# Optimization experiments

Hardware: AMD Instinct MI355X
Metric: run time of the kernel (lower is better)

Reference implementation:

```python
import jax, jax.numpy as jnp
import numpy as np

K1, K2, K3 = 6, 4, 3  # knn_graph k (loop=True -> self included, dist 0 is always top)


def _sqdist(a, b):
    # a: [B,N,3], b: [B,M,3] -> [B,N,M] squared euclidean distances
    an = jnp.sum(a * a, -1)[:, :, None]
    bn = jnp.sum(b * b, -1)[:, None, :]
    return an + bn - 2.0 * jnp.einsum('bnd,bmd->bnm', a, b)


def _knn_idx(pos, k):
    # for each point, indices of its k nearest neighbors (self included, loop=True)
    d = _sqdist(pos, pos)                 # [B,N,N]
    _, idx = jax.lax.top_k(-d, k)         # [B,N,k]
    return idx


def _gather(a, idx):
    # a: [B,N,...], idx: [B,...] -> per-cloud gather
    return jax.vmap(lambda ab, ib: ab[ib])(a, idx)


def _fps(pos, m):
    # farthest point sampling on one cloud [N,3], deterministic start at index 0
    min_d = jnp.sum((pos - pos[0]) ** 2, -1)  # [N]

    def step(min_d, _):
        idx = jnp.argmax(min_d)
        d = jnp.sum((pos - pos[idx]) ** 2, -1)
        return jnp.minimum(min_d, d), idx

    _, idxs = jax.lax.scan(step, min_d, None, length=m - 1)
    return jnp.concatenate([jnp.zeros((1,), dtype=idxs.dtype), idxs])


def _pn_layer(h, pos, k, W1, b1, W2, b2):
    # PointNetLayer: gather h_i/h_j/pos_i/pos_j over knn edges, MLP, max-aggregate
    idx = _knn_idx(pos, k)                       # [B,N,k]
    h_j = _gather(h, idx)                        # [B,N,k,C]
    pos_j = _gather(pos, idx)                    # [B,N,k,3]
    rel = pos_j - pos[:, :, None, :]             # pos_j - pos_i
    h_i = jnp.broadcast_to(h[:, :, None, :], h_j.shape)
    inp = jnp.concatenate([h_i, h_j, rel], -1)   # [B,N,k,2C+3]
    msg = jnp.maximum(inp @ W1 + b1, 0.0) @ W2 + b2
    return jnp.max(msg, axis=2)                  # scatter-max == dense max over k


def _forward(x, pos, W11, b11, W12, b12, W21, b21, W22, b22, W31, b31, W32, b32, Wr, br):
    h = jax.nn.relu(_pn_layer(x, pos, K1, W11, b11, W12, b12))
    idx = jax.vmap(lambda p: _fps(p, p.shape[0] // 2))(pos)   # ratio=0.5
    pos, h = _gather(pos, idx), _gather(h, idx)
    h = jax.nn.relu(_pn_layer(h, pos, K2, W21, b21, W22, b22))
    idx = jax.vmap(lambda p: _fps(p, p.shape[0] // 2))(pos)
    pos, h = _gather(pos, idx), _gather(h, idx)
    h = jax.nn.relu(_pn_layer(h, pos, K3, W31, b31, W32, b32))
    g = jnp.max(h, axis=1)                        # global_max_pool
    return g @ Wr + br                            # [B,10]


def _lin(key, fin, fout):
    k1, k2 = jax.random.split(key)
    lim = 1.0 / np.sqrt(fin)
    W = jax.random.uniform(k1, (fin, fout), minval=-lim, maxval=lim, dtype=jnp.float32)
    b = jax.random.uniform(k2, (fout,), minval=-lim, maxval=lim, dtype=jnp.float32)
    return W, b


def setup_inputs() -> dict:
    key = jax.random.key(0)
    ks = jax.random.split(key, 10)
    B, N = 16, 4096
    x = jax.random.normal(ks[0], (B, N, 1), dtype=jnp.float32)
    pos = jax.random.uniform(ks[1], (B, N, 3), dtype=jnp.float32)
    W11, b11 = _lin(ks[2], 1 * 2 + 3, 32)
    W12, b12 = _lin(ks[3], 32, 32)
    W21, b21 = _lin(ks[4], 32 * 2 + 3, 32)
    W22, b22 = _lin(ks[5], 32, 32)
    W31, b31 = _lin(ks[6], 32 * 2 + 3, 32)
    W32, b32 = _lin(ks[7], 32, 32)
    Wr, br = _lin(ks[8], 32, 10)
    return dict(x=x, pos=pos, W11=W11, b11=b11, W12=W12, b12=b12,
                W21=W21, b21=b21, W22=W22, b22=b22,
                W31=W31, b31=b31, W32=W32, b32=b32, Wr=Wr, br=br)


def reference(x, pos, W11, b11, W12, b12, W21, b21, W22, b22, W31, b31, W32, b32, Wr, br):
    return _forward(x, pos, W11, b11, W12, b12, W21, b21, W22, b22,
                    W31, b31, W32, b32, Wr, br)
```

## Files before the change

### kernel.cpp

```cpp
#include <hip/hip_runtime.h>

#define BATCH 16
#define NP1 4096
#define NP2 2048
#define NP3 1024

typedef float v2f __attribute__((ext_vector_type(2)));

__device__ __forceinline__ float f_add(float a, float b) { return __fadd_rn(a, b); }
__device__ __forceinline__ float f_mul(float a, float b) { return __fmul_rn(a, b); }
__device__ __forceinline__ float f_sub(float a, float b) { return __fsub_rn(a, b); }
__device__ __forceinline__ float sqnorm3(float x, float y, float z) {
  return f_add(f_add(f_mul(x, x), f_mul(y, y)), f_mul(z, z));
}

__device__ __forceinline__ unsigned long long u64max(unsigned long long a,
                                                     unsigned long long b) {
  return a > b ? a : b;
}
__device__ __forceinline__ unsigned long long u64min(unsigned long long a,
                                                     unsigned long long b) {
  return a < b ? a : b;
}
__device__ __forceinline__ double dmax(double a, double b) { return __builtin_fmax(a, b); }
__device__ __forceinline__ double dmin(double a, double b) { return __builtin_fmin(a, b); }

template<int CTRL, int RMASK>
__device__ __forceinline__ unsigned long long dpp_u64(unsigned long long k) {
  const int lo = __builtin_amdgcn_update_dpp(0, (int)(unsigned)k, CTRL, RMASK, 0xF, true);
  const int hi = __builtin_amdgcn_update_dpp(0, (int)(unsigned)(k >> 32), CTRL, RMASK, 0xF, true);
  return ((unsigned long long)(unsigned)hi << 32) | (unsigned)lo;
}
template<int CTRL, int RMASK>
__device__ __forceinline__ double dpp_dbl(double v) {
  return __longlong_as_double(
      (long long)dpp_u64<CTRL, RMASK>((unsigned long long)__double_as_longlong(v)));
}


__device__ __forceinline__ void tup_comb(double& a1, double& a2, double b1, double b2) {
  const double hi = dmax(a1, b1);
  const double lo = dmin(a1, b1);
  a2 = dmax(lo, dmax(a2, b2));
  a1 = hi;
}
template<int CTRL, int RMASK>
__device__ __forceinline__ void tup_stage(double& a1, double& a2) {
  const double b1 = dpp_dbl<CTRL, RMASK>(a1);
  const double b2 = dpp_dbl<CTRL, RMASK>(a2);
  tup_comb(a1, a2, b1, b2);
}

template<int N, int M>
__device__ void fps_block(char* __restrict__ smem, const float* __restrict__ P,
                          int* __restrict__ samp, float* __restrict__ pos_out)
{
#pragma clang fp contract(off)
  constexpr int THREADS = 512;
  constexpr int E = N / THREADS;
  constexpr int P2 = E / 2;
  float4* pos4 = (float4*)smem;
  unsigned short* ord = (unsigned short*)(smem + 16 * N);
  int* sampL = (int*)(smem + 18 * N);
  unsigned* cursor = (unsigned*)(smem + 18 * N + 4 * M);
  double* kslots = (double*)(smem + 18 * N + 4 * M + 32);
  const int tid = threadIdx.x;
  const int lane = tid & 63, wv = tid >> 6;
  const int myslot = lane & 7;
  if (tid < 8) cursor[tid] = 0u;
  __syncthreads();
  int oct[E];
#pragma unroll
  for (int e = 0; e < E; ++e) {
    const int t = e * THREADS + tid;
    const float x = P[t * 3], y = P[t * 3 + 1], z = P[t * 3 + 2];
    pos4[t] = make_float4(x, y, z, 0.f);
    oct[e] = (x > 0.5f ? 1 : 0) | (y > 0.5f ? 2 : 0) | (z > 0.5f ? 4 : 0);
    atomicAdd(&cursor[oct[e]], 1u);
  }
  __syncthreads();
  if (tid == 0) {
    unsigned run = 0;
#pragma unroll
    for (int o = 0; o < 8; ++o) { const unsigned c = cursor[o]; cursor[o] = run; run += c; }
  }
  __syncthreads();
#pragma unroll
  for (int e = 0; e < E; ++e) {
    const unsigned d = atomicAdd(&cursor[oct[e]], 1u);
    ord[d] = (unsigned short)(e * THREADS + tid);
  }
  __syncthreads();
  const float4 p0 = pos4[0];
  const float x0 = p0.x, y0 = p0.y, z0 = p0.z;
  v2f X2[P2], Y2[P2], Z2[P2], MD2[P2];
  unsigned ILO[E];
  float mnx = 1e30f, mny = 1e30f, mnz = 1e30f;
  float mxx = -1e30f, mxy = -1e30f, mxz = -1e30f;
  {
    const v2f x0v = {x0, x0}, y0v = {y0, y0}, z0v = {z0, z0};
#pragma unroll
    for (int p = 0; p < P2; ++p) {
      const int q0 = wv * (64 * E) + (2 * p) * 64 + lane;
      const int o0 = ord[q0], o1 = ord[q0 + 64];
      const float4 a0 = pos4[o0], a1 = pos4[o1];
      X2[p] = (v2f){a0.x, a1.x}; Y2[p] = (v2f){a0.y, a1.y}; Z2[p] = (v2f){a0.z, a1.z};
      mnx = fminf(mnx, fminf(a0.x, a1.x)); mxx = fmaxf(mxx, fmaxf(a0.x, a1.x));
      mny = fminf(mny, fminf(a0.y, a1.y)); mxy = fmaxf(mxy, fmaxf(a0.y, a1.y));
      mnz = fminf(mnz, fminf(a0.z, a1.z)); mxz = fmaxf(mxz, fmaxf(a0.z, a1.z));
      const v2f dx = X2[p] - x0v, dy = Y2[p] - y0v, dz = Z2[p] - z0v;
      MD2[p] = (dx * dx + dy * dy) + dz * dz;
      ILO[2 * p]     = 0xFFFFFFFFu - (unsigned)o0;
      ILO[2 * p + 1] = 0xFFFFFFFFu - (unsigned)o1;
    }
  }
#pragma unroll
  for (int off = 1; off < 64; off <<= 1) {
    mnx = fminf(mnx, __shfl_xor(mnx, off)); mxx = fmaxf(mxx, __shfl_xor(mxx, off));
    mny = fminf(mny, __shfl_xor(mny, off)); mxy = fmaxf(mxy, __shfl_xor(mxy, off));
    mnz = fminf(mnz, __shfl_xor(mnz, off)); mxz = fmaxf(mxz, __shfl_xor(mxz, off));
  }
  if (tid == 0) sampL[0] = 0;
  bool dirty = true;
  double W1 = 0.0, W2 = 0.0;
  int s = 1, it = 0;
#pragma unroll 1
  while (s < M) {
    if (dirty) {
      double k[E];
#pragma unroll
      for (int p = 0; p < P2; ++p) {
        k[2 * p] = __longlong_as_double((long long)(
            ((unsigned long long)__float_as_uint(MD2[p].x) << 32) | ILO[2 * p]));
        k[2 * p + 1] = __longlong_as_double((long long)(
            ((unsigned long long)__float_as_uint(MD2[p].y) << 32) | ILO[2 * p + 1]));
      }
      double A1 = dmax(k[0], k[1]), A2 = dmin(k[0], k[1]);
      double B1 = dmax(k[2], k[3]), B2 = dmin(k[2], k[3]);
      double C1 = dmax(k[4], k[5]), C2 = dmin(k[4], k[5]);
      double D1 = dmax(k[6], k[7]), D2 = dmin(k[6], k[7]);
      tup_comb(A1, A2, B1, B2); tup_comb(C1, C2, D1, D2); tup_comb(A1, A2, C1, C2);
      tup_stage<0x111, 0xF>(A1, A2);
      tup_stage<0x112, 0xF>(A1, A2);
      tup_stage<0x114, 0xF>(A1, A2);
      tup_stage<0x118, 0xF>(A1, A2);
      tup_stage<0x142, 0xA>(A1, A2);
      tup_stage<0x143, 0xC>(A1, A2);
      W1 = A1; W2 = A2;
    }
    const int pb = it & 1;
    if (lane == 63) ((double2*)kslots)[pb * 8 + wv] = make_double2(W1, W2);
    __syncthreads();
    double2 tt = ((double2*)kslots)[pb * 8 + myslot];
    double T1 = tt.x, T2 = tt.y;
    tup_stage<0xB1, 0xF>(T1, T2);
    tup_stage<0x4E, 0xF>(T1, T2);
    tup_stage<0x124, 0xF>(T1, T2);
    const unsigned long long g1b = (unsigned long long)__double_as_longlong(T1);
    const unsigned long long g2b = (unsigned long long)__double_as_longlong(T2);
    const int gi1 = (int)(0xFFFFFFFFu - (unsigned)g1b);
    const int gi2 = (int)(0xFFFFFFFFu - (unsigned)g2b);
    const float4 sp1 = pos4[gi1];
    const float4 sp2 = pos4[gi2];
    const float md2b = __uint_as_float((unsigned)(g2b >> 32));
    const float ddx = f_sub(sp2.x, sp1.x), ddy = f_sub(sp2.y, sp1.y),
                ddz = f_sub(sp2.z, sp1.z);
    const float dchk = f_add(f_add(f_mul(ddx, ddx), f_mul(ddy, ddy)), f_mul(ddz, ddz));
    const bool take2 = (s + 1 < M) && (dchk >= md2b);
    if (tid == 0) { sampL[s] = gi1; if (take2) sampL[s + 1] = gi2; }
    const float wmaxf = __uint_as_float((unsigned)__builtin_amdgcn_readlane(
        (int)(unsigned)((unsigned long long)__double_as_longlong(W1) >> 32), 63));
    const float m1x = fmaxf(fmaxf(f_sub(mnx, sp1.x), f_sub(sp1.x, mxx)), 0.f);
    const float m1y = fmaxf(fmaxf(f_sub(mny, sp1.y), f_sub(sp1.y, mxy)), 0.f);
    const float m1z = fmaxf(fmaxf(f_sub(mnz, sp1.z), f_sub(sp1.z, mxz)), 0.f);
    const bool u1 = sqnorm3(m1x, m1y, m1z) < wmaxf;
    const float m2x = fmaxf(fmaxf(f_sub(mnx, sp2.x), f_sub(sp2.x, mxx)), 0.f);
    const float m2y = fmaxf(fmaxf(f_sub(mny, sp2.y), f_sub(sp2.y, mxy)), 0.f);
    const float m2z = fmaxf(fmaxf(f_sub(mnz, sp2.z), f_sub(sp2.z, mxz)), 0.f);
    const bool u2 = take2 && (sqnorm3(m2x, m2y, m2z) < wmaxf);
    if (u1 | u2) {
      dirty = true;
      if (u1 & u2) {
        const v2f s1x = {sp1.x, sp1.x}, s1y = {sp1.y, sp1.y}, s1z = {sp1.z, sp1.z};
        const v2f s2x = {sp2.x, sp2.x}, s2y = {sp2.y, sp2.y}, s2z = {sp2.z, sp2.z};
#pragma unroll
        for (int p = 0; p < P2; ++p) {
          const v2f dx1 = X2[p] - s1x, dy1 = Y2[p] - s1y, dz1 = Z2[p] - s1z;
          const v2f d1 = (dx1 * dx1 + dy1 * dy1) + dz1 * dz1;
          MD2[p] = __builtin_elementwise_min(MD2[p], d1);
          const v2f dx2 = X2[p] - s2x, dy2 = Y2[p] - s2y, dz2 = Z2[p] - s2z;
          const v2f d2 = (dx2 * dx2 + dy2 * dy2) + dz2 * dz2;
          MD2[p] = __builtin_elementwise_min(MD2[p], d2);
        }
      } else {
        const float4 sp = u1 ? sp1 : sp2;
        const v2f sxv = {sp.x, sp.x}, syv = {sp.y, sp.y}, szv = {sp.z, sp.z};
#pragma unroll
        for (int p = 0; p < P2; ++p) {
          const v2f dx = X2[p] - sxv, dy = Y2[p] - syv, dz = Z2[p] - szv;
          const v2f d = (dx * dx + dy * dy) + dz * dz;
          MD2[p] = __builtin_elementwise_min(MD2[p], d);
        }
      }
    } else {
      dirty = false;
    }
    s += take2 ? 2 : 1;
    ++it;
  }
  __syncthreads();
  for (int s2 = tid; s2 < M; s2 += THREADS) {
    const int g = sampL[s2];
    samp[s2] = g;
    const float4 sp2 = pos4[g];
    pos_out[3 * s2 + 0] = sp2.x;
    pos_out[3 * s2 + 1] = sp2.y;
    pos_out[3 * s2 + 2] = sp2.z;
  }
}

__device__ __forceinline__ float f4c(const float4& v, int c) {
  return c == 0 ? v.x : c == 1 ? v.y : c == 2 ? v.z : v.w;
}
__device__ __forceinline__ void fma4(float4& a, float v, const float4& w) {
  a.x += v * w.x; a.y += v * w.y; a.z += v * w.z; a.w += v * w.w;
}

template<int K, int C>
__device__ void pn_compute(
    const float4* __restrict__ sW1, const float4* __restrict__ sW2,
    const float* __restrict__ sb1, const float* __restrict__ sb2,
    const float* __restrict__ P, const float* __restrict__ Hsrc,
    const int* __restrict__ hmap, int i, float xi, float yi, float zi,
    const int* kn, float* __restrict__ outrow)
{
  float4 abase[8];
#pragma unroll
  for (int o = 0; o < 8; ++o)
    abase[o] = make_float4(sb1[4 * o], sb1[4 * o + 1], sb1[4 * o + 2], sb1[4 * o + 3]);
  if constexpr (C == 1) {
    const float v = Hsrc[hmap ? hmap[i] : i];
#pragma unroll
    for (int o = 0; o < 8; ++o) fma4(abase[o], v, sW1[o]);
  } else {
    const int ri = hmap ? hmap[i] : i;
    const float4* Hi = (const float4*)(Hsrc + (size_t)ri * C);
#pragma unroll
    for (int c4 = 0; c4 < C / 4; ++c4) {
      const float4 hv = Hi[c4];
#pragma unroll
      for (int q = 0; q < 4; ++q) {
        const float v = f4c(hv, q);
#pragma unroll
        for (int o = 0; o < 8; ++o) fma4(abase[o], v, sW1[(4 * c4 + q) * 8 + o]);
      }
    }
  }
  float4 best[8];
#pragma unroll
  for (int o = 0; o < 8; ++o)
    best[o] = make_float4(-__builtin_inff(), -__builtin_inff(), -__builtin_inff(), -__builtin_inff());

  auto edge_pair = [&](int j0, int j1) {
    float4 a0[8], a1[8];
#pragma unroll
    for (int o = 0; o < 8; ++o) { a0[o] = abase[o]; a1[o] = abase[o]; }
    const float rx0 = P[j0 * 3] - xi, ry0 = P[j0 * 3 + 1] - yi, rz0 = P[j0 * 3 + 2] - zi;
    const float rx1 = P[j1 * 3] - xi, ry1 = P[j1 * 3 + 1] - yi, rz1 = P[j1 * 3 + 2] - zi;
    if constexpr (C == 1) {
      const float v0 = Hsrc[hmap ? hmap[j0] : j0], v1 = Hsrc[hmap ? hmap[j1] : j1];
#pragma unroll
      for (int o = 0; o < 8; ++o) {
        const float4 w = sW1[C * 8 + o];
        fma4(a0[o], v0, w); fma4(a1[o], v1, w);
      }
    } else {
      const int r0i = hmap ? hmap[j0] : j0, r1i = hmap ? hmap[j1] : j1;
      const float4* Hj0 = (const float4*)(Hsrc + (size_t)r0i * C);
      const float4* Hj1 = (const float4*)(Hsrc + (size_t)r1i * C);
#pragma unroll
      for (int c4 = 0; c4 < C / 4; ++c4) {
        const float4 h0 = Hj0[c4], h1 = Hj1[c4];
#pragma unroll
        for (int q = 0; q < 4; ++q) {
          const float v0 = f4c(h0, q), v1 = f4c(h1, q);
#pragma unroll
          for (int o = 0; o < 8; ++o) {
            const float4 w = sW1[(C + 4 * c4 + q) * 8 + o];
            fma4(a0[o], v0, w); fma4(a1[o], v1, w);
          }
        }
      }
    }
    const float r0[3] = {rx0, ry0, rz0}, r1[3] = {rx1, ry1, rz1};
#pragma unroll
    for (int r = 0; r < 3; ++r) {
#pragma unroll
      for (int o = 0; o < 8; ++o) {
        const float4 w = sW1[(2 * C + r) * 8 + o];
        fma4(a0[o], r0[r], w); fma4(a1[o], r1[r], w);
      }
    }
#pragma unroll
    for (int o = 0; o < 8; ++o) {
      a0[o].x = fmaxf(a0[o].x, 0.f); a0[o].y = fmaxf(a0[o].y, 0.f);
      a0[o].z = fmaxf(a0[o].z, 0.f); a0[o].w = fmaxf(a0[o].w, 0.f);
      a1[o].x = fmaxf(a1[o].x, 0.f); a1[o].y = fmaxf(a1[o].y, 0.f);
      a1[o].z = fmaxf(a1[o].z, 0.f); a1[o].w = fmaxf(a1[o].w, 0.f);
    }
#pragma unroll
    for (int hf = 0; hf < 2; ++hf) {
      float4 m0[4], m1[4];
#pragma unroll
      for (int o4 = 0; o4 < 4; ++o4) {
        const int c0 = 16 * hf + 4 * o4;
        m0[o4] = make_float4(sb2[c0], sb2[c0 + 1], sb2[c0 + 2], sb2[c0 + 3]);
        m1[o4] = m0[o4];
      }
#pragma unroll
      for (int c = 0; c < 32; ++c) {
        const float v0 = f4c(a0[c >> 2], c & 3), v1 = f4c(a1[c >> 2], c & 3);
#pragma unroll
        for (int o4 = 0; o4 < 4; ++o4) {
          const float4 w = sW2[c * 8 + hf * 4 + o4];
          fma4(m0[o4], v0, w); fma4(m1[o4], v1, w);
        }
      }
#pragma unroll
      for (int o4 = 0; o4 < 4; ++o4) {
        float4& bb = best[hf * 4 + o4];
        bb.x = fmaxf(bb.x, fmaxf(m0[o4].x, m1[o4].x));
        bb.y = fmaxf(bb.y, fmaxf(m0[o4].y, m1[o4].y));
        bb.z = fmaxf(bb.z, fmaxf(m0[o4].z, m1[o4].z));
        bb.w = fmaxf(bb.w, fmaxf(m0[o4].w, m1[o4].w));
      }
    }
  };

#pragma unroll
  for (int e = 0; e + 1 < K; e += 2) edge_pair(kn[e], kn[e + 1]);

  float4* ho = (float4*)outrow;
#pragma unroll
  for (int o = 0; o < 8; ++o)
    ho[o] = make_float4(fmaxf(best[o].x, 0.0f), fmaxf(best[o].y, 0.0f),
                        fmaxf(best[o].z, 0.0f), fmaxf(best[o].w, 0.0f));
}

template<int K, int NC, int C, int THREADS>
__device__ void fused_knn_pn(char* __restrict__ smem,
    const float* __restrict__ P, const float* __restrict__ Hsrc,
    const int* __restrict__ hmap,
    const float* __restrict__ W1, const float* __restrict__ b1,
    const float* __restrict__ W2, const float* __restrict__ b2,
    float* __restrict__ hout, int s)
{
  constexpr int CIN = 2 * C + 3;
  float4* tile = (float4*)smem;
  float4* sW1 = (float4*)(smem + 16 * 1024);
  float4* sW2 = sW1 + CIN * 8;
  float* sb1 = (float*)(sW2 + 32 * 8);
  float* sb2 = sb1 + 32;
  const int tid = threadIdx.x;
  for (int t = tid; t < CIN * 8; t += THREADS) sW1[t] = ((const float4*)W1)[t];
  for (int t = tid; t < 32 * 8; t += THREADS) sW2[t] = ((const float4*)W2)[t];
  if (tid < 32) { sb1[tid] = b1[tid]; sb2[tid] = b2[tid]; }

  const float xi = P[s * 3], yi = P[s * 3 + 1], zi = P[s * 3 + 2];
  const float ni = sqnorm3(xi, yi, zi);
  float bd[K]; int bj[K];
#pragma unroll
  for (int t = 0; t < K; ++t) { bd[t] = __builtin_inff(); bj[t] = 0; }
  for (int base = 0; base < NC; base += 1024) {
    __syncthreads();
    for (int t = tid; t < 1024; t += THREADS) {
      const float* q = P + (size_t)(base + t) * 3;
      const float x = q[0], y = q[1], z = q[2];
      tile[t] = make_float4(x, y, z, sqnorm3(x, y, z));
    }
    __syncthreads();
#pragma unroll 1
    for (int t = 0; t < 1024; t += 8) {
      float dv[8];
#pragma unroll
      for (int u = 0; u < 8; ++u) {
        const float4 q = tile[t + u];
        const float dot = f_add(f_add(f_mul(xi, q.x), f_mul(yi, q.y)), f_mul(zi, q.z));
        dv[u] = f_sub(f_add(ni, q.w), f_mul(2.0f, dot));
      }
#pragma unroll
      for (int u = 0; u < 8; ++u) {
        if (dv[u] < bd[K - 1]) {
          bd[K - 1] = dv[u]; bj[K - 1] = base + t + u;
#pragma unroll
          for (int r = K - 1; r > 0; --r) {
            if (bd[r] < bd[r - 1]) {
              float td = bd[r]; bd[r] = bd[r - 1]; bd[r - 1] = td;
              int   tj = bj[r]; bj[r] = bj[r - 1]; bj[r - 1] = tj;
            } else break;
          }
        }
      }
    }
  }
  pn_compute<K, C>(sW1, sW2, sb1, sb2, P, Hsrc, hmap, s, xi, yi, zi, bj,
                   hout + (size_t)s * 32);
}

template<int K, int NC>
__device__ void fused_knn_pn_quad(char* __restrict__ smem,
    const float* __restrict__ P, const float* __restrict__ Hsrc,
    const int* __restrict__ hmap,
    const float* __restrict__ W1, const float* __restrict__ b1,
    const float* __restrict__ W2, const float* __restrict__ b2,
    float* __restrict__ hout, int s, int q)
{
  constexpr int THREADS = 256;
  constexpr int RQ = NC / 4;
  constexpr int CIN = 67;
  float4* tile = (float4*)smem;
  float4* sW1 = (float4*)(smem + 16 * (NC + 4));
  float4* sW2 = sW1 + CIN * 8;
  float* sb1 = (float*)(sW2 + 32 * 8);
  float* sb2 = sb1 + 32;
  const int tid = threadIdx.x;

  for (int t = tid; t < NC; t += THREADS) {
    const float* c = P + (size_t)t * 3;
    const float x = c[0], y = c[1], z = c[2];
    tile[t + t / RQ] = make_float4(x, y, z, sqnorm3(x, y, z));
  }
  for (int t = tid; t < CIN * 8; t += THREADS) sW1[t] = ((const float4*)W1)[t];
  for (int t = tid; t < 32 * 8; t += THREADS) sW2[t] = ((const float4*)W2)[t];
  if (tid < 32) { sb1[tid] = b1[tid]; sb2[tid] = b2[tid]; }
  __syncthreads();

  const float4 qv = tile[s + s / RQ];
  const float xi = qv.x, yi = qv.y, zi = qv.z, ni = qv.w;

  const int ri = hmap ? hmap[s] : s;
  float4 hi4[8];
  {
    const float4* Hi = (const float4*)(Hsrc + (size_t)ri * 32);
#pragma unroll
    for (int c4 = 0; c4 < 8; ++c4) hi4[c4] = Hi[c4];
  }

  float bd[4]; int bj[4];
#pragma unroll
  for (int t = 0; t < 4; ++t) { bd[t] = __builtin_inff(); bj[t] = 0; }
  const int sbase = q * (RQ + 1);
#pragma unroll 1
  for (int t = 0; t < RQ; t += 8) {
    float dv[8];
#pragma unroll
    for (int u = 0; u < 8; ++u) {
      const float4 c = tile[sbase + t + u];
      const float dot = f_add(f_add(f_mul(xi, c.x), f_mul(yi, c.y)), f_mul(zi, c.z));
      dv[u] = f_sub(f_add(ni, c.w), f_mul(2.0f, dot));
    }
#pragma unroll
    for (int u = 0; u < 8; ++u) {
      if (dv[u] < bd[3]) {
        bd[3] = dv[u]; bj[3] = q * RQ + t + u;
#pragma unroll
        for (int r = 3; r > 0; --r) {
          if (bd[r] < bd[r - 1]) {
            float td = bd[r]; bd[r] = bd[r - 1]; bd[r - 1] = td;
            int   tj = bj[r]; bj[r] = bj[r - 1]; bj[r - 1] = tj;
          } else break;
        }
      }
    }
  }
  unsigned long long a0, a1, a2, a3;
  {
    auto mk = [](float d, int j) {
      unsigned u = __float_as_uint(d);
      u ^= (unsigned)((int)u >> 31) | 0x80000000u;
      return ((unsigned long long)u << 32) | (unsigned)j;
    };
    a0 = mk(bd[0], bj[0]); a1 = mk(bd[1], bj[1]);
    a2 = mk(bd[2], bj[2]); a3 = mk(bd[3], bj[3]);
  }
  {
    const unsigned long long b0 = __shfl_xor(a0, 1), b1_ = __shfl_xor(a1, 1),
                             b2_ = __shfl_xor(a2, 1), b3_ = __shfl_xor(a3, 1);
    const unsigned long long t0 = u64min(a0, b3_), t1 = u64min(a1, b2_),
                             t2 = u64min(a2, b1_), t3 = u64min(a3, b0);
    const unsigned long long u0 = u64min(t0, t2), u2 = u64max(t0, t2),
                             u1 = u64min(t1, t3), u3 = u64max(t1, t3);
    a0 = u64min(u0, u1); a1 = u64max(u0, u1);
    a2 = u64min(u2, u3); a3 = u64max(u2, u3);
  }
  {
    const unsigned long long b0 = __shfl_xor(a0, 2), b1_ = __shfl_xor(a1, 2),
                             b2_ = __shfl_xor(a2, 2), b3_ = __shfl_xor(a3, 2);
    const unsigned long long t0 = u64min(a0, b3_), t1 = u64min(a1, b2_),
                             t2 = u64min(a2, b1_), t3 = u64min(a3, b0);
    const unsigned long long u0 = u64min(t0, t2), u2 = u64max(t0, t2),
                             u1 = u64min(t1, t3), u3 = u64max(t1, t3);
    a0 = u64min(u0, u1); a1 = u64max(u0, u1);
    a2 = u64min(u2, u3); a3 = u64max(u2, u3);
  }
  const int e = (q < K) ? q : (K - 1);
  const unsigned long long ke = (e == 0) ? a0 : (e == 1) ? a1 : (e == 2) ? a2 : a3;
  const int jn = (int)(unsigned)ke;

  const int rj = hmap ? hmap[jn] : jn;
  float4 hj4[8];
  {
    const float4* Hj = (const float4*)(Hsrc + (size_t)rj * 32);
#pragma unroll
    for (int c4 = 0; c4 < 8; ++c4) hj4[c4] = Hj[c4];
  }
  float4 acc[8];
#pragma unroll
  for (int o = 0; o < 8; ++o)
    acc[o] = make_float4(sb1[4 * o], sb1[4 * o + 1], sb1[4 * o + 2], sb1[4 * o + 3]);
#pragma unroll
  for (int c4 = 0; c4 < 8; ++c4) {
    const float4 hv = hi4[c4];
#pragma unroll
    for (int t = 0; t < 4; ++t) {
      const float v = f4c(hv, t);
#pragma unroll
      for (int o = 0; o < 8; ++o) fma4(acc[o], v, sW1[(4 * c4 + t) * 8 + o]);
    }
  }
#pragma unroll
  for (int c4 = 0; c4 < 8; ++c4) {
    const float4 hv = hj4[c4];
#pragma unroll
    for (int t = 0; t < 4; ++t) {
      const float v = f4c(hv, t);
#pragma unroll
      for (int o = 0; o < 8; ++o) fma4(acc[o], v, sW1[(32 + 4 * c4 + t) * 8 + o]);
    }
  }
  const float4 cj = tile[jn + jn / RQ];
  const float r3[3] = {cj.x - xi, cj.y - yi, cj.z - zi};
#pragma unroll
  for (int r = 0; r < 3; ++r)
#pragma unroll
    for (int o = 0; o < 8; ++o) fma4(acc[o], r3[r], sW1[(64 + r) * 8 + o]);
#pragma unroll
  for (int o = 0; o < 8; ++o) {
    acc[o].x = fmaxf(acc[o].x, 0.f); acc[o].y = fmaxf(acc[o].y, 0.f);
    acc[o].z = fmaxf(acc[o].z, 0.f); acc[o].w = fmaxf(acc[o].w, 0.f);
  }
  float4 m[8];
#pragma unroll
  for (int o = 0; o < 8; ++o)
    m[o] = make_float4(sb2[4 * o], sb2[4 * o + 1], sb2[4 * o + 2], sb2[4 * o + 3]);
#pragma unroll
  for (int c = 0; c < 32; ++c) {
    const float v = f4c(acc[c >> 2], c & 3);
#pragma unroll
    for (int o = 0; o < 8; ++o) fma4(m[o], v, sW2[c * 8 + o]);
  }
#pragma unroll
  for (int o = 0; o < 8; ++o) {
    float4 v = m[o];
    v.x = fmaxf(v.x, __shfl_xor(v.x, 1)); v.y = fmaxf(v.y, __shfl_xor(v.y, 1));
    v.z = fmaxf(v.z, __shfl_xor(v.z, 1)); v.w = fmaxf(v.w, __shfl_xor(v.w, 1));
    v.x = fmaxf(v.x, __shfl_xor(v.x, 2)); v.y = fmaxf(v.y, __shfl_xor(v.y, 2));
    v.z = fmaxf(v.z, __shfl_xor(v.z, 2)); v.w = fmaxf(v.w, __shfl_xor(v.w, 2));
    m[o] = v;
  }
  float4* ho = (float4*)(hout + (size_t)s * 32);
  {
    const float4 v0 = m[2 * q], v1 = m[2 * q + 1];
    ho[2 * q] = make_float4(fmaxf(v0.x, 0.f), fmaxf(v0.y, 0.f),
                            fmaxf(v0.z, 0.f), fmaxf(v0.w, 0.f));
    ho[2 * q + 1] = make_float4(fmaxf(v1.x, 0.f), fmaxf(v1.y, 0.f),
                                fmaxf(v1.z, 0.f), fmaxf(v1.w, 0.f));
  }
}

__global__ __launch_bounds__(512) void megaA(
    const float* __restrict__ x, const float* __restrict__ pos,
    const float* __restrict__ W11, const float* __restrict__ b11,
    const float* __restrict__ W12, const float* __restrict__ b12,
    int* __restrict__ samp1, float* __restrict__ pos2, float* __restrict__ h1full)
{
  __shared__ __align__(16) char smem[82240];
  if (blockIdx.x < BATCH) {
    const int b = blockIdx.x;
    fps_block<NP1, NP2>(smem, pos + (size_t)b * NP1 * 3, samp1 + b * NP2,
                        pos2 + (size_t)b * NP2 * 3);
  } else {
    const int id = blockIdx.x - BATCH;
    const int b = id >> 3;
    const int s = (id & 7) * 512 + threadIdx.x;
    fused_knn_pn<6, NP1, 1, 512>(smem, pos + (size_t)b * NP1 * 3, x + (size_t)b * NP1,
                                 nullptr, W11, b11, W12, b12,
                                 h1full + (size_t)b * NP1 * 32, s);
  }
}

__global__ __launch_bounds__(256) void megaB(
    const float* __restrict__ pos2, const int* __restrict__ samp1,
    const float* __restrict__ h1full,
    const float* __restrict__ W21, const float* __restrict__ b21,
    const float* __restrict__ W22, const float* __restrict__ b22,
    float* __restrict__ h2out)
{
  __shared__ __align__(16) char smem[(2048 + 4) * 16 + 67 * 8 * 16 + 32 * 8 * 16 + 256];
  const int b = blockIdx.x >> 4;
  const int s = ((blockIdx.x & 15) << 6) + (threadIdx.x >> 2);
  const int q = threadIdx.x & 3;
  fused_knn_pn_quad<4, NP2>(smem, pos2 + (size_t)b * NP2 * 3,
                            h1full + (size_t)b * NP1 * 32, samp1 + b * NP2,
                            W21, b21, W22, b22, h2out + (size_t)b * NP3 * 32, s, q);
}

__global__ __launch_bounds__(256) void megaC(
    const float* __restrict__ pos2, const float* __restrict__ h2out,
    const float* __restrict__ W31, const float* __restrict__ b31,
    const float* __restrict__ W32, const float* __restrict__ b32,
    float* __restrict__ h3full)
{
  __shared__ __align__(16) char smem[(1024 + 4) * 16 + 67 * 8 * 16 + 32 * 8 * 16 + 256];
  const int b = blockIdx.x >> 4;
  const int s = ((blockIdx.x & 15) << 6) + (threadIdx.x >> 2);
  const int q = threadIdx.x & 3;
  fused_knn_pn_quad<3, NP3>(smem, pos2 + (size_t)b * NP2 * 3,
                            h2out + (size_t)b * NP3 * 32, nullptr,
                            W31, b31, W32, b32, h3full + (size_t)b * NP3 * 32, s, q);
}

__global__ __launch_bounds__(256) void final_kernel(
    const float* __restrict__ h, const float* __restrict__ Wr,
    const float* __restrict__ br, float* __restrict__ out)
{
  __shared__ float red[8][32];
  __shared__ float g[32];
  const int b = blockIdx.x;
  const int c = threadIdx.x & 31, grp = threadIdx.x >> 5;
  const float* H = h + (size_t)b * NP3 * 32;
  float m = -__builtin_inff();
  for (int r = grp; r < NP3; r += 8) m = fmaxf(m, H[r * 32 + c]);
  red[grp][c] = m;
  __syncthreads();
  if (threadIdx.x < 32) {
    float v = red[0][c];
#pragma unroll
    for (int w = 1; w < 8; ++w) v = fmaxf(v, red[w][c]);
    g[c] = v;
  }
  __syncthreads();
  if (threadIdx.x < 10) {
    float v = br[threadIdx.x];
#pragma unroll
    for (int cc = 0; cc < 32; ++cc) v += g[cc] * Wr[cc * 10 + threadIdx.x];
    out[b * 10 + threadIdx.x] = v;
  }
}

extern "C" void kernel_launch(void* const* d_in, const int* in_sizes, int n_in,
                              void* d_out, int out_size, void* d_ws, size_t ws_size,
                              hipStream_t stream) {
  const float* x   = (const float*)d_in[0];
  const float* pos = (const float*)d_in[1];
  const float* W11 = (const float*)d_in[2];
  const float* b11 = (const float*)d_in[3];
  const float* W12 = (const float*)d_in[4];
  const float* b12 = (const float*)d_in[5];
  const float* W21 = (const float*)d_in[6];
  const float* b21 = (const float*)d_in[7];
  const float* W22 = (const float*)d_in[8];
  const float* b22 = (const float*)d_in[9];
  const float* W31 = (const float*)d_in[10];
  const float* b31 = (const float*)d_in[11];
  const float* W32 = (const float*)d_in[12];
  const float* b32 = (const float*)d_in[13];
  const float* Wr  = (const float*)d_in[14];
  const float* br  = (const float*)d_in[15];
  float* out = (float*)d_out;

  char* p = (char*)d_ws;
  auto alloc = [&](size_t bytes) {
    char* r = p; p += (bytes + 255) & ~(size_t)255; return r;
  };
  int*   samp1  = (int*)  alloc(sizeof(int)   * BATCH * NP2);
  float* pos2   = (float*)alloc(sizeof(float) * BATCH * NP2 * 3);
  float* h1full = (float*)alloc(sizeof(float) * BATCH * NP1 * 32);
  float* h2out  = (float*)alloc(sizeof(float) * BATCH * NP3 * 32);
  float* h3full = (float*)alloc(sizeof(float) * BATCH * NP3 * 32);

  megaA<<<BATCH + BATCH * (NP1 / 512), 512, 0, stream>>>(
      x, pos, W11, b11, W12, b12, samp1, pos2, h1full);
  megaB<<<BATCH * 16, 256, 0, stream>>>(
      pos2, samp1, h1full, W21, b21, W22, b22, h2out);
  megaC<<<BATCH * 16, 256, 0, stream>>>(
      pos2, h2out, W31, b31, W32, b32, h3full);
  final_kernel<<<BATCH, 256, 0, stream>>>(h3full, Wr, br, out);
}
```

Measured before the change: 1.325 ms.

## Track top-3 keys in FPS reduction to accept second sample more often

The farthest-point-sampling reduction now keeps the top three packed (distance,index) keys instead of two, through the per-thread, DPP and cross-wave stages. The second candidate is accepted when its distance, updated against the first pick, still beats the third key, rather than only when its distance to the first pick exceeds its own min-distance. The aim is to take two samples per iteration more often, which cuts the number of serial barrier-bound iterations. The cost is roughly 50% more DPP and min/max work per reduction, plus a larger shared slot area.

```diff
diff --git a/kernel.cpp b/kernel.cpp
--- a/kernel.cpp
+++ b/kernel.cpp
@@ -38,17 +38,29 @@
 }
 
 
-__device__ __forceinline__ void tup_comb(double& a1, double& a2, double b1, double b2) {
-  const double hi = dmax(a1, b1);
-  const double lo = dmin(a1, b1);
-  a2 = dmax(lo, dmax(a2, b2));
-  a1 = hi;
+__device__ __forceinline__ void tup3_comb(double& a1, double& a2, double& a3,
+                                          double b1, double b2, double b3) {
+  const double r1 = dmax(a1, b1);
+  const double m1 = dmin(a1, b1);
+  const double M2 = dmax(a2, b2);
+  const double r2 = dmax(m1, M2);
+  const double r3 = dmax(dmin(M2, m1), dmax(a3, b3));
+  a1 = r1; a2 = r2; a3 = r3;
 }
 template<int CTRL, int RMASK>
-__device__ __forceinline__ void tup_stage(double& a1, double& a2) {
+__device__ __forceinline__ void tup3_stage(double& a1, double& a2, double& a3) {
   const double b1 = dpp_dbl<CTRL, RMASK>(a1);
   const double b2 = dpp_dbl<CTRL, RMASK>(a2);
-  tup_comb(a1, a2, b1, b2);
+  const double b3 = dpp_dbl<CTRL, RMASK>(a3);
+  tup3_comb(a1, a2, a3, b1, b2, b3);
+}
+__device__ __forceinline__ void comb22to3(double p1, double p2, double q1, double q2,
+                                          double& o1, double& o2, double& o3) {
+  o1 = dmax(p1, q1);
+  const double m1 = dmin(p1, q1);
+  const double M2 = dmax(p2, q2);
+  o2 = dmax(m1, M2);
+  o3 = dmin(m1, M2);
 }
 
 template<int N, int M>
@@ -122,7 +134,7 @@
   }
   if (tid == 0) sampL[0] = 0;
   bool dirty = true;
-  double W1 = 0.0, W2 = 0.0;
+  double W1 = 0.0, W2 = 0.0, W3 = 0.0;
   int s = 1, it = 0;
 #pragma unroll 1
   while (s < M) {
@@ -135,29 +147,38 @@
         k[2 * p + 1] = __longlong_as_double((long long)(
             ((unsigned long long)__float_as_uint(MD2[p].y) << 32) | ILO[2 * p + 1]));
       }
-      double A1 = dmax(k[0], k[1]), A2 = dmin(k[0], k[1]);
-      double B1 = dmax(k[2], k[3]), B2 = dmin(k[2], k[3]);
-      double C1 = dmax(k[4], k[5]), C2 = dmin(k[4], k[5]);
-      double D1 = dmax(k[6], k[7]), D2 = dmin(k[6], k[7]);
-      tup_comb(A1, A2, B1, B2); tup_comb(C1, C2, D1, D2); tup_comb(A1, A2, C1, C2);
-      tup_stage<0x111, 0xF>(A1, A2);
-      tup_stage<0x112, 0xF>(A1, A2);
-      tup_stage<0x114, 0xF>(A1, A2);
-      tup_stage<0x118, 0xF>(A1, A2);
-      tup_stage<0x142, 0xA>(A1, A2);
-      tup_stage<0x143, 0xC>(A1, A2);
-      W1 = A1; W2 = A2;
+      double h1[4], h2[4];
+#pragma unroll
+      for (int i = 0; i < 4; ++i) {
+        h1[i] = dmax(k[2 * i], k[2 * i + 1]);
+        h2[i] = dmin(k[2 * i], k[2 * i + 1]);
+      }
+      double A1, A2, A3, B1, B2, B3;
+      comb22to3(h1[0], h2[0], h1[1], h2[1], A1, A2, A3);
+      comb22to3(h1[2], h2[2], h1[3], h2[3], B1, B2, B3);
+      tup3_comb(A1, A2, A3, B1, B2, B3);
+      tup3_stage<0x111, 0xF>(A1, A2, A3);
+      tup3_stage<0x112, 0xF>(A1, A2, A3);
+      tup3_stage<0x114, 0xF>(A1, A2, A3);
+      tup3_stage<0x118, 0xF>(A1, A2, A3);
+      tup3_stage<0x142, 0xA>(A1, A2, A3);
+      tup3_stage<0x143, 0xC>(A1, A2, A3);
+      W1 = A1; W2 = A2; W3 = A3;
     }
     const int pb = it & 1;
-    if (lane == 63) ((double2*)kslots)[pb * 8 + wv] = make_double2(W1, W2);
+    if (lane == 63) {
+      double* sl = kslots + pb * 32 + wv * 4;
+      sl[0] = W1; sl[1] = W2; sl[2] = W3;
+    }
     __syncthreads();
-    double2 tt = ((double2*)kslots)[pb * 8 + myslot];
-    double T1 = tt.x, T2 = tt.y;
-    tup_stage<0xB1, 0xF>(T1, T2);
-    tup_stage<0x4E, 0xF>(T1, T2);
-    tup_stage<0x124, 0xF>(T1, T2);
+    const double* sl = kslots + pb * 32 + myslot * 4;
+    double T1 = sl[0], T2 = sl[1], T3 = sl[2];
+    tup3_stage<0xB1, 0xF>(T1, T2, T3);
+    tup3_stage<0x4E, 0xF>(T1, T2, T3);
+    tup3_stage<0x124, 0xF>(T1, T2, T3);
     const unsigned long long g1b = (unsigned long long)__double_as_longlong(T1);
     const unsigned long long g2b = (unsigned long long)__double_as_longlong(T2);
+    const unsigned long long g3b = (unsigned long long)__double_as_longlong(T3);
     const int gi1 = (int)(0xFFFFFFFFu - (unsigned)g1b);
     const int gi2 = (int)(0xFFFFFFFFu - (unsigned)g2b);
     const float4 sp1 = pos4[gi1];
@@ -166,7 +187,10 @@
     const float ddx = f_sub(sp2.x, sp1.x), ddy = f_sub(sp2.y, sp1.y),
                 ddz = f_sub(sp2.z, sp1.z);
     const float dchk = f_add(f_add(f_mul(ddx, ddx), f_mul(ddy, ddy)), f_mul(ddz, ddz));
-    const bool take2 = (s + 1 < M) && (dchk >= md2b);
+    const float nmd2 = fminf(md2b, dchk);
+    const unsigned long long nk2 =
+        ((unsigned long long)__float_as_uint(nmd2) << 32) | (unsigned)g2b;
+    const bool take2 = (s + 1 < M) && (nk2 > g3b);
     if (tid == 0) { sampL[s] = gi1; if (take2) sampL[s + 1] = gi2; }
     const float wmaxf = __uint_as_float((unsigned)__builtin_amdgcn_readlane(
         (int)(unsigned)((unsigned long long)__double_as_longlong(W1) >> 32), 63));
@@ -584,7 +608,7 @@
     const float* __restrict__ W12, const float* __restrict__ b12,
     int* __restrict__ samp1, float* __restrict__ pos2, float* __restrict__ h1full)
 {
-  __shared__ __align__(16) char smem[82240];
+  __shared__ __align__(16) char smem[82496];
   if (blockIdx.x < BATCH) {
     const int b = blockIdx.x;
     fps_block<NP1, NP2>(smem, pos + (size_t)b * NP1 * 3, samp1 + b * NP2,
```

Result: slower. 1.517 ms (+14.5%).
